# Kernel optimization log

Hardware: AMD Instinct MI355X
Metric: run time of the kernel (lower is better)

## Reference

```python
import jax, jax.numpy as jnp
import numpy as np

B, S, HID = 1, 4096, 1024
H, KV, D = 16, 4, 64           # heads, kv heads, head_dim
N_REP = H // KV
WINDOW = 512
EPS = 1e-5
ROPE_THETA = 1e6


def _rope_tables(seq_len, dim, theta):
    inv_freq = 1.0 / (theta ** (np.arange(0, dim, 2, dtype=np.float32) / dim))
    t = np.arange(seq_len, dtype=np.float32)
    freqs = np.outer(t, inv_freq)                      # [S, D/2]
    emb = np.concatenate([freqs, freqs], axis=-1)      # [S, D]
    return jnp.asarray(np.cos(emb)), jnp.asarray(np.sin(emb))


def setup_inputs() -> dict:
    key = jax.random.key(0)
    ks = jax.random.split(key, 7)
    cos, sin = _rope_tables(S, D, ROPE_THETA)
    return {
        "x": jax.random.normal(ks[0], (B, S, HID), jnp.float32),
        "cos": cos,
        "sin": sin,
        "wq": jax.random.normal(ks[1], (H * D, HID), jnp.float32) * (HID ** -0.5),
        "wk": jax.random.normal(ks[2], (KV * D, HID), jnp.float32) * (HID ** -0.5),
        "wv": jax.random.normal(ks[3], (KV * D, HID), jnp.float32) * (HID ** -0.5),
        "wo": jax.random.normal(ks[4], (HID, H * D), jnp.float32) * (HID ** -0.5),
        "q_norm_w": jnp.ones((D,), jnp.float32),
        "k_norm_w": jnp.ones((D,), jnp.float32),
        "sinks": jax.random.normal(ks[5], (H,), jnp.float32),
    }


def _rms_norm(v, w):
    return v * jax.lax.rsqrt(jnp.mean(v * v, axis=-1, keepdims=True) + EPS) * w


def _rotate_half(v):
    h = v.shape[-1] // 2
    return jnp.concatenate([-v[..., h:], v[..., :h]], axis=-1)


def reference(x, cos, sin, wq, wk, wv, wo, q_norm_w, k_norm_w, sinks):
    b, s, _ = x.shape
    q = (x @ wq.T).reshape(b, s, H, D)
    k = (x @ wk.T).reshape(b, s, KV, D)
    v = (x @ wv.T).reshape(b, s, KV, D)
    q = _rms_norm(q, q_norm_w)
    k = _rms_norm(k, k_norm_w)
    c = cos[:, None, :]  # [s,1,d] broadcast over heads
    sn = sin[:, None, :]
    q = q * c + _rotate_half(q) * sn
    k = k * c + _rotate_half(k) * sn
    # GQA: repeat kv heads
    k = jnp.repeat(k, N_REP, axis=2)  # [b,s,H,D]
    v = jnp.repeat(v, N_REP, axis=2)
    scores = jnp.einsum("bqhd,bkhd->bhqk", q, k) / np.sqrt(D)  # [b,H,s,s]
    i = jnp.arange(s)[:, None]
    j = jnp.arange(s)[None, :]
    allowed = (j <= i) & (j > i - WINDOW)  # causal + sliding window
    scores = jnp.where(allowed, scores, -jnp.inf)
    # append per-head learned sink logit, softmax in fp32, then drop sink col
    sink = jnp.broadcast_to(sinks.reshape(1, H, 1, 1), (b, H, s, 1))
    attn = jax.nn.softmax(jnp.concatenate([scores, sink], axis=-1).astype(jnp.float32), axis=-1)
    attn = attn[..., :-1].astype(q.dtype)
    out = jnp.einsum("bhqk,bkhd->bqhd", attn, v).reshape(b, s, H * D)
    return out @ wo.T
```

## Files before the change

### kernel.cpp

```cpp
#include <hip/hip_runtime.h>
#include <hip/hip_bf16.h>
#include <stdint.h>

#define S_LEN   4096
#define HIDDEN  1024
#define NHEAD   16
#define NKV     4
#define HD      64
#define WINDOW  512
#define L2E     1.4426950408889634f
#define QSCALE  (0.125f * L2E)

using short8 = __attribute__((ext_vector_type(8))) short;
using f32x4  = __attribute__((ext_vector_type(4))) float;
using f32x16 = __attribute__((ext_vector_type(16))) float;

__device__ __forceinline__ uint16_t f2bf(float f) {
  uint32_t u = __builtin_bit_cast(uint32_t, f);
  u += 0x7fffu + ((u >> 16) & 1u);
  return (uint16_t)(u >> 16);
}
__device__ __forceinline__ uint16_t f2bf_rn(float f) {
  uint32_t u = __builtin_bit_cast(uint32_t, f);
  return (uint16_t)((u + 0x8000u) >> 16);
}
__device__ __forceinline__ uint32_t pk2(float a, float b) {
  return (uint32_t)f2bf_rn(a) | ((uint32_t)f2bf_rn(b) << 16);
}

__device__ __forceinline__ void gld_lds16(void* lds, const void* g) {
  __builtin_amdgcn_global_load_lds(
      (const __attribute__((address_space(1))) char*)g,
      (__attribute__((address_space(3))) char*)lds, 16, 0, 0);
}

__global__ __launch_bounds__(256) void k_tobf16(
    const float* __restrict__ x, const float* __restrict__ wq,
    const float* __restrict__ wk, const float* __restrict__ wv,
    const float* __restrict__ wo,
    uint16_t* __restrict__ xb, uint16_t* __restrict__ wqkvb,
    uint16_t* __restrict__ wob) {
  int i = blockIdx.x * 256 + threadIdx.x;
  const float4* src; uint16_t* dst; int off;
  if (i < 1048576)      { src = (const float4*)x;  dst = xb;                off = i; }
  else if (i < 1310720) { src = (const float4*)wq; dst = wqkvb;             off = i - 1048576; }
  else if (i < 1376256) { src = (const float4*)wk; dst = wqkvb + 1024*1024; off = i - 1310720; }
  else if (i < 1441792) { src = (const float4*)wv; dst = wqkvb + 1280*1024; off = i - 1376256; }
  else                  { src = (const float4*)wo; dst = wob;               off = i - 1441792; }
  float4 v = src[off];
  ushort4 o = { f2bf(v.x), f2bf(v.y), f2bf(v.z), f2bf(v.w) };
  *(ushort4*)(dst + (size_t)off * 4) = o;
}

__global__ __launch_bounds__(256) void k_gemm_qkv(
    const uint16_t* __restrict__ A, const uint16_t* __restrict__ B,
    const float* __restrict__ cosb, const float* __restrict__ sinb,
    const float* __restrict__ qw, const float* __restrict__ kw,
    uint16_t* __restrict__ qout, uint16_t* __restrict__ kout,
    uint16_t* __restrict__ vtout) {
  __shared__ uint16_t As[64 * 64];
  __shared__ uint16_t Bs[128 * 64];
  const int K = 1024;
  const int t = threadIdx.x;
  const int lane = t & 63, w = t >> 6;
  const int wr = w >> 1, wc = w & 1;
  const int l16 = lane & 15, lg = lane >> 4;
  const int bm = blockIdx.x, bn = blockIdx.y;
  const uint16_t* Ab = A + (size_t)bm * 64 * K;
  const uint16_t* Bb = B + (size_t)bn * 128 * K;
  f32x4 acc[2][4] = {};
  for (int k0 = 0; k0 < K; k0 += 64) {
    __syncthreads();
    {
      int row = t >> 3, c8 = (t & 7) << 3;
      gld_lds16(&As[t * 8], Ab + (size_t)row * K + k0 + c8);
      int t2 = t + 256, row2 = t2 >> 3, c82 = (t2 & 7) << 3;
      gld_lds16(&As[t2 * 8], Ab + (size_t)row2 * K + k0 + c82);
    }
#pragma unroll
    for (int it = 0; it < 4; ++it) {
      int idx = it * 256 + t;
      int row = idx >> 3, c8 = (idx & 7) << 3;
      gld_lds16(&Bs[idx * 8], Bb + (size_t)row * K + k0 + c8);
    }
    __syncthreads();
#pragma unroll
    for (int kk = 0; kk < 2; ++kk) {
      short8 af[2], bq[4];
#pragma unroll
      for (int i = 0; i < 2; ++i)
        af[i] = *(const short8*)&As[(wr * 32 + i * 16 + l16) * 64 + kk * 32 + lg * 8];
#pragma unroll
      for (int j = 0; j < 4; ++j)
        bq[j] = *(const short8*)&Bs[(wc * 64 + j * 16 + l16) * 64 + kk * 32 + lg * 8];
#pragma unroll
      for (int i = 0; i < 2; ++i)
#pragma unroll
        for (int j = 0; j < 4; ++j)
          acc[i][j] = __builtin_amdgcn_mfma_f32_16x16x32_bf16(af[i], bq[j], acc[i][j], 0, 0, 0);
    }
  }

  const int hg = bn * 2 + wc;
  if (hg >= 20) {
    const int kvh = hg - 20;
#pragma unroll
    for (int i = 0; i < 2; ++i) {
      int row0 = bm * 64 + wr * 32 + i * 16 + lg * 4;
#pragma unroll
      for (int j = 0; j < 4; ++j) {
        int d = j * 16 + l16;
        ushort4 o = { f2bf(acc[i][j][0]), f2bf(acc[i][j][1]),
                      f2bf(acc[i][j][2]), f2bf(acc[i][j][3]) };
        *(ushort4*)(vtout + (size_t)(kvh * 64 + d) * S_LEN + row0) = o;
      }
    }
    return;
  }
  const float* nw = (hg < 16) ? qw : kw;
  float wgt[4];
#pragma unroll
  for (int j = 0; j < 4; ++j) wgt[j] = nw[j * 16 + l16];
#pragma unroll
  for (int i = 0; i < 2; ++i) {
    int row0 = bm * 64 + wr * 32 + i * 16 + lg * 4;
    float qn[4][4];
#pragma unroll
    for (int r = 0; r < 4; ++r) {
      float ss = acc[i][0][r] * acc[i][0][r] + acc[i][1][r] * acc[i][1][r]
               + acc[i][2][r] * acc[i][2][r] + acc[i][3][r] * acc[i][3][r];
      ss += __shfl_xor(ss, 1);
      ss += __shfl_xor(ss, 2);
      ss += __shfl_xor(ss, 4);
      ss += __shfl_xor(ss, 8);
      float inv = rsqrtf(ss * (1.0f / 64.0f) + 1e-5f);
#pragma unroll
      for (int j = 0; j < 4; ++j) qn[j][r] = acc[i][j][r] * inv * wgt[j];
    }
#pragma unroll
    for (int j = 0; j < 4; ++j) {
      int d = j * 16 + l16;
#pragma unroll
      for (int r = 0; r < 4; ++r) {
        int row = row0 + r;
        float rot = (j < 2) ? -qn[j + 2][r] : qn[j - 2][r];
        float o = qn[j][r] * cosb[row * 64 + d] + rot * sinb[row * 64 + d];
        if (hg < 16)
          qout[(size_t)row * HIDDEN + hg * 64 + d] = f2bf(o * QSCALE);
        else
          kout[((size_t)(hg - 16) * S_LEN + row) * 64 + d] = f2bf(o);
      }
    }
  }
}

__global__ __launch_bounds__(256) void k_gemm_bf16(
    const uint16_t* __restrict__ A, const uint16_t* __restrict__ B,
    float* __restrict__ C, int N, int K) {
  __shared__ uint16_t As[64 * 64];
  __shared__ uint16_t Bs[128 * 64];
  const int t = threadIdx.x;
  const int lane = t & 63, w = t >> 6;
  const int wr = w >> 1, wc = w & 1;
  const int l16 = lane & 15, lg = lane >> 4;
  const int bm = blockIdx.x, bn = blockIdx.y;
  const uint16_t* Ab = A + (size_t)bm * 64 * K;
  const uint16_t* Bb = B + (size_t)bn * 128 * K;
  f32x4 acc[2][4] = {};
  for (int k0 = 0; k0 < K; k0 += 64) {
    __syncthreads();
    {
      int row = t >> 3, c8 = (t & 7) << 3;
      gld_lds16(&As[t * 8], Ab + (size_t)row * K + k0 + c8);
      int t2 = t + 256, row2 = t2 >> 3, c82 = (t2 & 7) << 3;
      gld_lds16(&As[t2 * 8], Ab + (size_t)row2 * K + k0 + c82);
    }
#pragma unroll
    for (int it = 0; it < 4; ++it) {
      int idx = it * 256 + t;
      int row = idx >> 3, c8 = (idx & 7) << 3;
      gld_lds16(&Bs[idx * 8], Bb + (size_t)row * K + k0 + c8);
    }
    __syncthreads();
#pragma unroll
    for (int kk = 0; kk < 2; ++kk) {
      short8 af[2], bq[4];
#pragma unroll
      for (int i = 0; i < 2; ++i)
        af[i] = *(const short8*)&As[(wr * 32 + i * 16 + l16) * 64 + kk * 32 + lg * 8];
#pragma unroll
      for (int j = 0; j < 4; ++j)
        bq[j] = *(const short8*)&Bs[(wc * 64 + j * 16 + l16) * 64 + kk * 32 + lg * 8];
#pragma unroll
      for (int i = 0; i < 2; ++i)
#pragma unroll
        for (int j = 0; j < 4; ++j)
          acc[i][j] = __builtin_amdgcn_mfma_f32_16x16x32_bf16(af[i], bq[j], acc[i][j], 0, 0, 0);
    }
  }
#pragma unroll
  for (int i = 0; i < 2; ++i) {
    int row0 = bm * 64 + wr * 32 + i * 16 + lg * 4;
#pragma unroll
    for (int j = 0; j < 4; ++j) {
      int col = bn * 128 + wc * 64 + j * 16 + l16;
#pragma unroll
      for (int r = 0; r < 4; ++r)
        C[(size_t)(row0 + r) * N + col] = acc[i][j][r];
    }
  }
}

__global__ __launch_bounds__(256) void k_attn(
    const uint16_t* __restrict__ qb,
    const uint16_t* __restrict__ kb,
    const uint16_t* __restrict__ vtb,
    const float* __restrict__ sinks,
    uint16_t* __restrict__ ao) {
  const int t = threadIdx.x;
  const int lane = t & 63, w = t >> 6;
  const int linear = blockIdx.x + 64 * blockIdx.y;
  const int lid = (linear & 7) * 64 + (linear >> 3);
  const int q0 = (63 - (lid & 63)) * 64;
  const int hp = lid >> 6;
  const int kvh = hp >> 1;
  const int h = kvh * 4 + (hp & 1) * 2 + (w >> 1);
  const int qbase = q0 + (w & 1) * 32;
  const int l32 = lane & 31, hi = lane >> 5;
  const int qrow = qbase + l32;

  short8 bq[4];
  {
    const uint16_t* qp = qb + (size_t)qrow * HIDDEN + h * 64 + hi * 8;
    bq[0] = *(const short8*)(qp);
    bq[1] = *(const short8*)(qp + 16);
    bq[2] = *(const short8*)(qp + 32);
    bq[3] = *(const short8*)(qp + 48);
  }
  const uint16_t* kbase = kb + (size_t)kvh * S_LEN * 64;
  const uint16_t* vbase = vtb + (size_t)kvh * 64 * S_LEN;

  f32x16 acc0 = {}, acc1 = {};
  float lsum = 0.f;
  int kstart = q0 - WINDOW;
  if (kstart < 0) kstart = 0;

  for (int k0 = kstart; k0 <= q0; k0 += 64) {
    const bool edge = (k0 == q0) || (k0 == q0 - WINDOW);
    const uint16_t* kt = kbase + (size_t)(k0 + l32) * 64 + hi * 8;
#pragma unroll
    for (int c = 0; c < 2; ++c) {
      f32x16 st = {};
#pragma unroll
      for (int s = 0; s < 4; ++s) {
        short8 ak = *(const short8*)(kt + c * 32 * 64 + s * 16);
        st = __builtin_amdgcn_mfma_f32_32x32x16_bf16(ak, bq[s], st, 0, 0, 0);
      }
      float pp[16];
      if (edge) {
#pragma unroll
        for (int r = 0; r < 16; ++r) {
          int key = k0 + c * 32 + 4 * hi + (r & 3) + 8 * (r >> 2);
          bool ok = (key <= qrow) && (key + WINDOW > qrow);
          pp[r] = ok ? exp2f(st[r]) : 0.f;
        }
      } else {
#pragma unroll
        for (int r = 0; r < 16; ++r) pp[r] = exp2f(st[r]);
      }
#pragma unroll
      for (int r = 0; r < 16; ++r) lsum += pp[r];
      uint32_t wvp[8];
#pragma unroll
      for (int i = 0; i < 8; ++i) wvp[i] = pk2(pp[2 * i], pp[2 * i + 1]);
#pragma unroll
      for (int half = 0; half < 2; ++half) {
        uint32_t x0 = wvp[half * 4 + 0], x1 = wvp[half * 4 + 1];
        uint32_t x2 = wvp[half * 4 + 2], x3 = wvp[half * 4 + 3];
        uint32_t p0 = (uint32_t)__shfl_xor((int)x0, 32);
        uint32_t p1 = (uint32_t)__shfl_xor((int)x1, 32);
        uint32_t p2 = (uint32_t)__shfl_xor((int)x2, 32);
        uint32_t p3 = (uint32_t)__shfl_xor((int)x3, 32);
        uint4 au = { hi ? p2 : x0, hi ? p3 : x1, hi ? x2 : p0, hi ? x3 : p1 };
        short8 pa = __builtin_bit_cast(short8, au);
        const uint16_t* vt = vbase + (size_t)l32 * S_LEN
                           + k0 + c * 32 + half * 16 + hi * 8;
        short8 bv0 = *(const short8*)(vt);
        short8 bv1 = *(const short8*)(vt + 32 * S_LEN);
        acc0 = __builtin_amdgcn_mfma_f32_32x32x16_bf16(pa, bv0, acc0, 0, 0, 0);
        acc1 = __builtin_amdgcn_mfma_f32_32x32x16_bf16(pa, bv1, acc1, 0, 0, 0);
      }
    }
  }

  lsum += __shfl_xor(lsum, 32);
  float inv = 1.0f / (lsum + exp2f(sinks[h] * L2E));
#pragma unroll
  for (int r = 0; r < 16; ++r) {
    int rloc = (r & 3) + 8 * (r >> 2) + 4 * hi;
    float rd = __shfl(inv, rloc);
    size_t base = (size_t)(qbase + rloc) * HIDDEN + h * 64 + l32;
    ao[base]      = f2bf(acc0[r] * rd);
    ao[base + 32] = f2bf(acc1[r] * rd);
  }
}

extern "C" void kernel_launch(void* const* d_in, const int* in_sizes, int n_in,
                              void* d_out, int out_size, void* d_ws, size_t ws_size,
                              hipStream_t stream) {
  const float* x     = (const float*)d_in[0];
  const float* cosb  = (const float*)d_in[1];
  const float* sinb  = (const float*)d_in[2];
  const float* wq    = (const float*)d_in[3];
  const float* wk    = (const float*)d_in[4];
  const float* wv    = (const float*)d_in[5];
  const float* wo    = (const float*)d_in[6];
  const float* qnw   = (const float*)d_in[7];
  const float* knw   = (const float*)d_in[8];
  const float* sinks = (const float*)d_in[9];
  float* out = (float*)d_out;

  char* ws = (char*)d_ws;
  uint16_t* xb    = (uint16_t*)(ws);
  uint16_t* wqkvb = (uint16_t*)(ws + (8ll  << 20));
  uint16_t* wob   = (uint16_t*)(ws + (11ll << 20));
  uint16_t* qsc   = (uint16_t*)(ws + (13ll << 20));
  uint16_t* kbf   = (uint16_t*)(ws + (21ll << 20));
  uint16_t* vtb   = (uint16_t*)(ws + (23ll << 20));
  uint16_t* aob   = (uint16_t*)(ws + (25ll << 20));

  k_tobf16  <<<6656, 256, 0, stream>>>(x, wq, wk, wv, wo, xb, wqkvb, wob);
  k_gemm_qkv<<<dim3(64, 12), 256, 0, stream>>>(xb, wqkvb, cosb, sinb, qnw, knw,
                                               qsc, kbf, vtb);
  k_attn    <<<dim3(64, 8), 256, 0, stream>>>(qsc, kbf, vtb, sinks, aob);
  k_gemm_bf16<<<dim3(64, 8), 256, 0, stream>>>(aob, wob, out, 1024, 1024);
}
```

Baseline: 96.72 us.

## Stage K/V tiles through double-buffered LDS with register prefetch in attention

```diff
diff --git a/kernel.cpp b/kernel.cpp
--- a/kernel.cpp
+++ b/kernel.cpp
@@ -217,13 +217,13 @@
     const uint16_t* __restrict__ vtb,
     const float* __restrict__ sinks,
     uint16_t* __restrict__ ao) {
+  __shared__ uint16_t Kl[2][64][72];
+  __shared__ uint16_t Vl[2][64][72];
+  const int q0 = (63 - blockIdx.x) * 64;
+  const int hp = blockIdx.y;
+  const int kvh = hp >> 1;
   const int t = threadIdx.x;
   const int lane = t & 63, w = t >> 6;
-  const int linear = blockIdx.x + 64 * blockIdx.y;
-  const int lid = (linear & 7) * 64 + (linear >> 3);
-  const int q0 = (63 - (lid & 63)) * 64;
-  const int hp = lid >> 6;
-  const int kvh = hp >> 1;
   const int h = kvh * 4 + (hp & 1) * 2 + (w >> 1);
   const int qbase = q0 + (w & 1) * 32;
   const int l32 = lane & 31, hi = lane >> 5;
@@ -237,25 +237,61 @@
     bq[2] = *(const short8*)(qp + 32);
     bq[3] = *(const short8*)(qp + 48);
   }
-  const uint16_t* kbase = kb + (size_t)kvh * S_LEN * 64;
-  const uint16_t* vbase = vtb + (size_t)kvh * 64 * S_LEN;
+
+  int kstart = q0 - WINDOW;
+  if (kstart < 0) kstart = 0;
+
+  const int r1 = t >> 3, sc8 = (t & 7) << 3;
+  const uint16_t* kp = kb + ((size_t)kvh * S_LEN + r1) * 64 + sc8;
+  const uint16_t* kp2 = kp + (size_t)32 * 64;
+  const uint16_t* vp = vtb + ((size_t)kvh * 64 + r1) * S_LEN + sc8;
+  const uint16_t* vp2 = vp + (size_t)32 * S_LEN;
+
+  short8 nk0 = *(const short8*)(kp  + (size_t)kstart * 64);
+  short8 nk1 = *(const short8*)(kp2 + (size_t)kstart * 64);
+  short8 nv0 = *(const short8*)(vp  + kstart);
+  short8 nv1 = *(const short8*)(vp2 + kstart);
+  *(short8*)&Kl[0][r1][sc8]      = nk0;
+  *(short8*)&Kl[0][r1 + 32][sc8] = nk1;
+  *(short8*)&Vl[0][r1][sc8]      = nv0;
+  *(short8*)&Vl[0][r1 + 32][sc8] = nv1;
+  if (kstart + 64 <= q0) {
+    nk0 = *(const short8*)(kp  + (size_t)(kstart + 64) * 64);
+    nk1 = *(const short8*)(kp2 + (size_t)(kstart + 64) * 64);
+    nv0 = *(const short8*)(vp  + kstart + 64);
+    nv1 = *(const short8*)(vp2 + kstart + 64);
+  }
+  __syncthreads();
 
   f32x16 acc0 = {}, acc1 = {};
   float lsum = 0.f;
-  int kstart = q0 - WINDOW;
-  if (kstart < 0) kstart = 0;
-
-  for (int k0 = kstart; k0 <= q0; k0 += 64) {
+  int ib = 0;
+
+  for (int k0 = kstart; k0 <= q0; k0 += 64, ib ^= 1) {
+    if (k0 + 64 <= q0) {
+      *(short8*)&Kl[ib ^ 1][r1][sc8]      = nk0;
+      *(short8*)&Kl[ib ^ 1][r1 + 32][sc8] = nk1;
+      *(short8*)&Vl[ib ^ 1][r1][sc8]      = nv0;
+      *(short8*)&Vl[ib ^ 1][r1 + 32][sc8] = nv1;
+      if (k0 + 128 <= q0) {
+        nk0 = *(const short8*)(kp  + (size_t)(k0 + 128) * 64);
+        nk1 = *(const short8*)(kp2 + (size_t)(k0 + 128) * 64);
+        nv0 = *(const short8*)(vp  + k0 + 128);
+        nv1 = *(const short8*)(vp2 + k0 + 128);
+      }
+    }
+
     const bool edge = (k0 == q0) || (k0 == q0 - WINDOW);
-    const uint16_t* kt = kbase + (size_t)(k0 + l32) * 64 + hi * 8;
 #pragma unroll
     for (int c = 0; c < 2; ++c) {
       f32x16 st = {};
+      __builtin_amdgcn_s_setprio(1);
 #pragma unroll
       for (int s = 0; s < 4; ++s) {
-        short8 ak = *(const short8*)(kt + c * 32 * 64 + s * 16);
+        short8 ak = *(const short8*)&Kl[ib][c * 32 + l32][s * 16 + hi * 8];
         st = __builtin_amdgcn_mfma_f32_32x32x16_bf16(ak, bq[s], st, 0, 0, 0);
       }
+      __builtin_amdgcn_s_setprio(0);
       float pp[16];
       if (edge) {
 #pragma unroll
@@ -283,14 +319,15 @@
         uint32_t p3 = (uint32_t)__shfl_xor((int)x3, 32);
         uint4 au = { hi ? p2 : x0, hi ? p3 : x1, hi ? x2 : p0, hi ? x3 : p1 };
         short8 pa = __builtin_bit_cast(short8, au);
-        const uint16_t* vt = vbase + (size_t)l32 * S_LEN
-                           + k0 + c * 32 + half * 16 + hi * 8;
-        short8 bv0 = *(const short8*)(vt);
-        short8 bv1 = *(const short8*)(vt + 32 * S_LEN);
+        short8 bv0 = *(const short8*)&Vl[ib][l32][c * 32 + half * 16 + hi * 8];
+        short8 bv1 = *(const short8*)&Vl[ib][32 + l32][c * 32 + half * 16 + hi * 8];
+        __builtin_amdgcn_s_setprio(1);
         acc0 = __builtin_amdgcn_mfma_f32_32x32x16_bf16(pa, bv0, acc0, 0, 0, 0);
         acc1 = __builtin_amdgcn_mfma_f32_32x32x16_bf16(pa, bv1, acc1, 0, 0, 0);
-      }
-    }
+        __builtin_amdgcn_s_setprio(0);
+      }
+    }
+    __syncthreads();
   }
 
   lsum += __shfl_xor(lsum, 32);
```

Measured after the change: 84.69 us. 1.14x faster.

## Stage K/V tiles in LDS, split key range across waves, remap GEMM blocks per XCD

Applied to the files above, without the earlier changes.

```diff
diff --git a/kernel.cpp b/kernel.cpp
--- a/kernel.cpp
+++ b/kernel.cpp
@@ -65,7 +65,10 @@
   const int lane = t & 63, w = t >> 6;
   const int wr = w >> 1, wc = w & 1;
   const int l16 = lane & 15, lg = lane >> 4;
-  const int bm = blockIdx.x, bn = blockIdx.y;
+  const int bid = blockIdx.x;
+  const int xcd = bid & 7, idx = bid >> 3;
+  const int bm = xcd + 8 * (idx & 7);
+  const int bn = idx >> 3;
   const uint16_t* Ab = A + (size_t)bm * 64 * K;
   const uint16_t* Bb = B + (size_t)bn * 128 * K;
   f32x4 acc[2][4] = {};
@@ -79,9 +82,9 @@
     }
 #pragma unroll
     for (int it = 0; it < 4; ++it) {
-      int idx = it * 256 + t;
-      int row = idx >> 3, c8 = (idx & 7) << 3;
-      gld_lds16(&Bs[idx * 8], Bb + (size_t)row * K + k0 + c8);
+      int idx2 = it * 256 + t;
+      int row = idx2 >> 3, c8 = (idx2 & 7) << 3;
+      gld_lds16(&Bs[idx2 * 8], Bb + (size_t)row * K + k0 + c8);
     }
     __syncthreads();
 #pragma unroll
@@ -163,7 +166,10 @@
   const int lane = t & 63, w = t >> 6;
   const int wr = w >> 1, wc = w & 1;
   const int l16 = lane & 15, lg = lane >> 4;
-  const int bm = blockIdx.x, bn = blockIdx.y;
+  const int bid = blockIdx.x;
+  const int xcd = bid & 7, idx = bid >> 3;
+  const int bm = xcd + 8 * (idx & 7);
+  const int bn = idx >> 3;
   const uint16_t* Ab = A + (size_t)bm * 64 * K;
   const uint16_t* Bb = B + (size_t)bn * 128 * K;
   f32x4 acc[2][4] = {};
@@ -177,9 +183,9 @@
     }
 #pragma unroll
     for (int it = 0; it < 4; ++it) {
-      int idx = it * 256 + t;
-      int row = idx >> 3, c8 = (idx & 7) << 3;
-      gld_lds16(&Bs[idx * 8], Bb + (size_t)row * K + k0 + c8);
+      int idx2 = it * 256 + t;
+      int row = idx2 >> 3, c8 = (idx2 & 7) << 3;
+      gld_lds16(&Bs[idx2 * 8], Bb + (size_t)row * K + k0 + c8);
     }
     __syncthreads();
 #pragma unroll
@@ -211,21 +217,26 @@
   }
 }
 
-__global__ __launch_bounds__(256) void k_attn(
+__global__ __launch_bounds__(512) void k_attn(
     const uint16_t* __restrict__ qb,
     const uint16_t* __restrict__ kb,
     const uint16_t* __restrict__ vtb,
     const float* __restrict__ sinks,
     uint16_t* __restrict__ ao) {
+  __shared__ __align__(16) char smem[36864];
+  auto Kl = (uint16_t(*)[64][72])(smem);
+  auto Vl = (uint16_t(*)[64][72])(smem + 18432);
+  float* Ms = (float*)smem;
+
+  const int bid = blockIdx.x;
+  const int hp = bid & 7;
+  const int q0 = (63 - (bid >> 3)) * 64;
+  const int kvh = hp >> 1;
   const int t = threadIdx.x;
   const int lane = t & 63, w = t >> 6;
-  const int linear = blockIdx.x + 64 * blockIdx.y;
-  const int lid = (linear & 7) * 64 + (linear >> 3);
-  const int q0 = (63 - (lid & 63)) * 64;
-  const int hp = lid >> 6;
-  const int kvh = hp >> 1;
-  const int h = kvh * 4 + (hp & 1) * 2 + (w >> 1);
-  const int qbase = q0 + (w & 1) * 32;
+  const int kh = w & 1, qs = (w >> 1) & 1, hd = w >> 2;
+  const int h = kvh * 4 + (hp & 1) * 2 + hd;
+  const int qbase = q0 + qs * 32;
   const int l32 = lane & 31, hi = lane >> 5;
   const int qrow = qbase + l32;
 
@@ -237,25 +248,64 @@
     bq[2] = *(const short8*)(qp + 32);
     bq[3] = *(const short8*)(qp + 48);
   }
-  const uint16_t* kbase = kb + (size_t)kvh * S_LEN * 64;
-  const uint16_t* vbase = vtb + (size_t)kvh * 64 * S_LEN;
+
+  int kstart = q0 - WINDOW;
+  if (kstart < 0) kstart = 0;
+  const int nt = ((q0 - kstart) >> 6) + 1;
+  const int n0 = nt >> 1;
+  const int n1 = nt - n0;
+
+  const int r1 = t >> 3, sc8 = (t & 7) << 3;
+  const uint16_t* kpb = kb + ((size_t)kvh * S_LEN + r1) * 64 + sc8;
+  const uint16_t* vpb = vtb + ((size_t)kvh * 64 + r1) * S_LEN + sc8;
+  short8 nk0, nv0, nk1, nv1;
+  if (n0 > 0) {
+    nk0 = *(const short8*)(kpb + (size_t)kstart * 64);
+    nv0 = *(const short8*)(vpb + kstart);
+  }
+  {
+    int kt1 = kstart + n0 * 64;
+    nk1 = *(const short8*)(kpb + (size_t)kt1 * 64);
+    nv1 = *(const short8*)(vpb + kt1);
+  }
 
   f32x16 acc0 = {}, acc1 = {};
   float lsum = 0.f;
-  int kstart = q0 - WINDOW;
-  if (kstart < 0) kstart = 0;
-
-  for (int k0 = kstart; k0 <= q0; k0 += 64) {
+
+  for (int s = 0; s < n1; ++s) {
+    __syncthreads();
+    if (s < n0) {
+      *(short8*)&Kl[0][r1][sc8] = nk0;
+      *(short8*)&Vl[0][r1][sc8] = nv0;
+    }
+    *(short8*)&Kl[1][r1][sc8] = nk1;
+    *(short8*)&Vl[1][r1][sc8] = nv1;
+    __syncthreads();
+    if (s + 1 < n0) {
+      int kt = kstart + (s + 1) * 64;
+      nk0 = *(const short8*)(kpb + (size_t)kt * 64);
+      nv0 = *(const short8*)(vpb + kt);
+    }
+    if (s + 1 < n1) {
+      int kt = kstart + (n0 + s + 1) * 64;
+      nk1 = *(const short8*)(kpb + (size_t)kt * 64);
+      nv1 = *(const short8*)(vpb + kt);
+    }
+
+    if (kh == 0 && s >= n0) continue;
+    const int k0 = kstart + (kh ? (n0 + s) : s) * 64;
     const bool edge = (k0 == q0) || (k0 == q0 - WINDOW);
-    const uint16_t* kt = kbase + (size_t)(k0 + l32) * 64 + hi * 8;
+
 #pragma unroll
     for (int c = 0; c < 2; ++c) {
       f32x16 st = {};
-#pragma unroll
-      for (int s = 0; s < 4; ++s) {
-        short8 ak = *(const short8*)(kt + c * 32 * 64 + s * 16);
-        st = __builtin_amdgcn_mfma_f32_32x32x16_bf16(ak, bq[s], st, 0, 0, 0);
+      __builtin_amdgcn_s_setprio(1);
+#pragma unroll
+      for (int s4 = 0; s4 < 4; ++s4) {
+        short8 ak = *(const short8*)&Kl[kh][c * 32 + l32][s4 * 16 + hi * 8];
+        st = __builtin_amdgcn_mfma_f32_32x32x16_bf16(ak, bq[s4], st, 0, 0, 0);
       }
+      __builtin_amdgcn_s_setprio(0);
       float pp[16];
       if (edge) {
 #pragma unroll
@@ -283,25 +333,41 @@
         uint32_t p3 = (uint32_t)__shfl_xor((int)x3, 32);
         uint4 au = { hi ? p2 : x0, hi ? p3 : x1, hi ? x2 : p0, hi ? x3 : p1 };
         short8 pa = __builtin_bit_cast(short8, au);
-        const uint16_t* vt = vbase + (size_t)l32 * S_LEN
-                           + k0 + c * 32 + half * 16 + hi * 8;
-        short8 bv0 = *(const short8*)(vt);
-        short8 bv1 = *(const short8*)(vt + 32 * S_LEN);
+        short8 bv0 = *(const short8*)&Vl[kh][l32][c * 32 + half * 16 + hi * 8];
+        short8 bv1 = *(const short8*)&Vl[kh][32 + l32][c * 32 + half * 16 + hi * 8];
+        __builtin_amdgcn_s_setprio(1);
         acc0 = __builtin_amdgcn_mfma_f32_32x32x16_bf16(pa, bv0, acc0, 0, 0, 0);
         acc1 = __builtin_amdgcn_mfma_f32_32x32x16_bf16(pa, bv1, acc1, 0, 0, 0);
+        __builtin_amdgcn_s_setprio(0);
       }
     }
   }
 
   lsum += __shfl_xor(lsum, 32);
-  float inv = 1.0f / (lsum + exp2f(sinks[h] * L2E));
-#pragma unroll
-  for (int r = 0; r < 16; ++r) {
-    int rloc = (r & 3) + 8 * (r >> 2) + 4 * hi;
-    float rd = __shfl(inv, rloc);
-    size_t base = (size_t)(qbase + rloc) * HIDDEN + h * 64 + l32;
-    ao[base]      = f2bf(acc0[r] * rd);
-    ao[base + 32] = f2bf(acc1[r] * rd);
+
+  __syncthreads();
+  const int pid = w >> 1;
+  if (kh == 1) {
+    float* m = &Ms[(size_t)(pid * 64 + lane) * 33];
+#pragma unroll
+    for (int r = 0; r < 16; ++r) { m[r] = acc0[r]; m[16 + r] = acc1[r]; }
+    m[32] = lsum;
+  }
+  __syncthreads();
+  if (kh == 0) {
+    const float* m = &Ms[(size_t)(pid * 64 + lane) * 33];
+#pragma unroll
+    for (int r = 0; r < 16; ++r) { acc0[r] += m[r]; acc1[r] += m[16 + r]; }
+    lsum += m[32];
+    float inv = 1.0f / (lsum + exp2f(sinks[h] * L2E));
+#pragma unroll
+    for (int r = 0; r < 16; ++r) {
+      int rloc = (r & 3) + 8 * (r >> 2) + 4 * hi;
+      float rd = __shfl(inv, rloc);
+      size_t base = (size_t)(qbase + rloc) * HIDDEN + h * 64 + l32;
+      ao[base]      = f2bf(acc0[r] * rd);
+      ao[base + 32] = f2bf(acc1[r] * rd);
+    }
   }
 }
 
@@ -330,8 +396,8 @@
   uint16_t* aob   = (uint16_t*)(ws + (25ll << 20));
 
   k_tobf16  <<<6656, 256, 0, stream>>>(x, wq, wk, wv, wo, xb, wqkvb, wob);
-  k_gemm_qkv<<<dim3(64, 12), 256, 0, stream>>>(xb, wqkvb, cosb, sinb, qnw, knw,
-                                               qsc, kbf, vtb);
-  k_attn    <<<dim3(64, 8), 256, 0, stream>>>(qsc, kbf, vtb, sinks, aob);
-  k_gemm_bf16<<<dim3(64, 8), 256, 0, stream>>>(aob, wob, out, 1024, 1024);
-}
+  k_gemm_qkv<<<768, 256, 0, stream>>>(xb, wqkvb, cosb, sinb, qnw, knw,
+                                      qsc, kbf, vtb);
+  k_attn    <<<512, 512, 0, stream>>>(qsc, kbf, vtb, sinks, aob);
+  k_gemm_bf16<<<512, 256, 0, stream>>>(aob, wob, out, 1024, 1024);
+}
```

Result: faster. 88.16 us (-8.9%).
